# Kernel optimization log

Hardware: AMD Instinct MI355X
Metric: run time of the kernel (lower is better)

The kernel has to match this reference:

```python
import jax, jax.numpy as jnp
import numpy as np

N_NODES = 50000
N_EDGES = 640000
IN_F, H1, H2, H3, N_CLS = 128, 128, 128, 128, 40


def setup_inputs() -> dict:
    key = jax.random.key(0)
    ks = jax.random.split(key, 16)
    def lin(k, i, o):
        bound = 1.0 / np.sqrt(i)
        kw, kb = jax.random.split(k)
        W = jax.random.uniform(kw, (i, o), jnp.float32, -bound, bound)
        b = jax.random.uniform(kb, (o,), jnp.float32, -bound, bound)
        return W, b
    Wr, br = lin(ks[0], IN_F, H3)
    W1, b1 = lin(ks[1], IN_F, H1)
    W2, b2 = lin(ks[2], H1, H2)
    W3, b3 = lin(ks[3], H2, H3)
    Wop, bop = lin(ks[4], H3, N_CLS)
    x = jax.random.normal(ks[5], (N_NODES, IN_F), jnp.float32)
    src = jax.random.randint(ks[6], (N_EDGES,), 0, N_NODES, jnp.int64)
    dst = jax.random.randint(ks[7], (N_EDGES,), 0, N_NODES, jnp.int64)
    edge_weight = jax.random.uniform(ks[8], (N_EDGES,), jnp.float32)
    return {"x": x, "src": src, "dst": dst, "edge_weight": edge_weight,
            "Wr": Wr, "br": br, "W1": W1, "b1": b1, "W2": W2, "b2": b2,
            "W3": W3, "b3": b3, "Wop": Wop, "bop": bop}


def _gconv(x, src, dst, ew, W, b, n_nodes):
    # gather neighbor features, scale by edge weight, scatter-sum to dst, linear
    msg = x[src] * ew[:, None]                      # [E, d_in]
    agg = jax.ops.segment_sum(msg, dst, num_segments=n_nodes)  # [N, d_in]
    return agg @ W + b


def reference(x, src, dst, edge_weight, Wr, br, W1, b1, W2, b2, W3, b3, Wop, bop):
    n = x.shape[0]
    res = x @ Wr + br
    h = jax.nn.relu(_gconv(x, src, dst, edge_weight, W1, b1, n))
    h = jax.nn.relu(_gconv(h, src, dst, edge_weight, W2, b2, n))
    h = _gconv(h, src, dst, edge_weight, W3, b3, n)
    h = jax.nn.relu(h + res)
    return h @ Wop + bop
```

## Files before the change

### kernel.cpp

```cpp
#include <hip/hip_runtime.h>
#include <hip/hip_fp16.h>
#include <stdint.h>


#define NF 128

typedef unsigned short u16;
typedef unsigned int u32;
typedef __attribute__((ext_vector_type(8))) short short8;
typedef __attribute__((ext_vector_type(4))) float f32x4;

__device__ __forceinline__ float bf2f(u16 v) {
    union { unsigned u; float f; } x; x.u = (unsigned)v << 16; return x.f;
}
__device__ __forceinline__ u16 f2bf(float f) {
    union { float f; unsigned u; } x; x.f = f;
    unsigned r = (x.u + 0x7FFFu + ((x.u >> 16) & 1u)) >> 16;
    return (u16)r;
}


__global__ __launch_bounds__(256) void hist_rank(
    const int* __restrict__ dst, int* __restrict__ counts,
    int* __restrict__ rank, int n_edges)
{
    int e = blockIdx.x * 256 + threadIdx.x;
    if (e < n_edges) rank[e] = atomicAdd(&counts[dst[e]], 1);
}

__global__ __launch_bounds__(256) void scan_pass1(
    const int* __restrict__ counts, int* __restrict__ bsums, int n)
{
    __shared__ int s[256];
    int i = blockIdx.x * 256 + threadIdx.x;
    s[threadIdx.x] = (i < n) ? counts[i] : 0;
    __syncthreads();
    for (int off = 128; off > 0; off >>= 1) {
        if (threadIdx.x < off) s[threadIdx.x] += s[threadIdx.x + off];
        __syncthreads();
    }
    if (threadIdx.x == 0) bsums[blockIdx.x] = s[0];
}

__global__ __launch_bounds__(256) void scan_pass2(int* __restrict__ bsums, int G)
{
    __shared__ int s[256];
    int t = threadIdx.x;
    int v = (t < G) ? bsums[t] : 0;
    s[t] = v;
    __syncthreads();
    for (int off = 1; off < 256; off <<= 1) {
        int u = (t >= off) ? s[t - off] : 0;
        __syncthreads();
        s[t] += u;
        __syncthreads();
    }
    if (t < G) bsums[t] = s[t] - v;
    if (t == 0) bsums[G] = s[255];
}

__global__ __launch_bounds__(256) void scan_pass3(
    int* __restrict__ rowptr, const int* __restrict__ bsums, int n, int G)
{
    __shared__ int s[256];
    int t = threadIdx.x;
    int i = blockIdx.x * 256 + t;
    int v = (i < n) ? rowptr[i] : 0;
    s[t] = v;
    __syncthreads();
    for (int off = 1; off < 256; off <<= 1) {
        int u = (t >= off) ? s[t - off] : 0;
        __syncthreads();
        s[t] += u;
        __syncthreads();
    }
    int excl = s[t] - v + bsums[blockIdx.x];
    if (i < n) rowptr[i] = excl;
    if (i == 0) rowptr[n] = bsums[G];
}

__global__ __launch_bounds__(256) void fill_packed(
    const int* __restrict__ src, const int* __restrict__ dst,
    const float* __restrict__ ew, const int* __restrict__ rowptr,
    const int* __restrict__ rank, u32* __restrict__ ppairs, int n_edges)
{
    int e = blockIdx.x * 256 + threadIdx.x;
    if (e >= n_edges) return;
    int pos = rowptr[dst[e]] + rank[e];
    ppairs[pos] = ((u32)src[e] << 16) |
                  (u32)__half_as_ushort(__float2half_rn(ew[e]));
}


__global__ __launch_bounds__(256) void cast_x_bf16(
    const float* __restrict__ in, u16* __restrict__ out, int n_elem)
{
    int idx = (blockIdx.x * 256 + threadIdx.x) * 4;
    if (idx >= n_elem) return;
    float4 v = *reinterpret_cast<const float4*>(in + idx);
    ushort4 o;
    o.x = f2bf(v.x); o.y = f2bf(v.y); o.z = f2bf(v.z); o.w = f2bf(v.w);
    *reinterpret_cast<ushort4*>(out + idx) = o;
}

__global__ __launch_bounds__(256) void prep_weights(
    const float* __restrict__ Wr, const float* __restrict__ W1,
    const float* __restrict__ W2, const float* __restrict__ W3,
    const float* __restrict__ Wop, u16* __restrict__ Wt, u16* __restrict__ Wtop)
{
    int i = blockIdx.x * 256 + threadIdx.x;
    if (i < 4 * 16384) {
        int w = i >> 14, r = i & 16383;
        int nn = r >> 7, kk = r & 127;
        const float* W = (w == 0) ? Wr : (w == 1) ? W1 : (w == 2) ? W2 : W3;
        Wt[i] = f2bf(W[kk * NF + nn]);
    } else {
        int r = i - 4 * 16384;
        if (r < 48 * 128) {
            int nn = r >> 7, kk = r & 127;
            Wtop[r] = (nn < 40) ? f2bf(Wop[kk * 40 + nn]) : (u16)0;
        }
    }
}

__global__ __launch_bounds__(256) void agg_gather_b(
    const u16* __restrict__ xb, const int* __restrict__ rowptr,
    const u32* __restrict__ ppairs, u16* __restrict__ aggb, int n_nodes)
{
    int gid = blockIdx.x * 256 + threadIdx.x;
    int node = gid >> 4;
    if (node >= n_nodes) return;
    int f = (gid & 15) << 3;
    int e0 = rowptr[node];
    int e1 = rowptr[node + 1];
    float acc[8];
    #pragma unroll
    for (int j = 0; j < 8; j++) acc[j] = 0.f;

    int e = e0;
    for (; e + 4 <= e1; e += 4) {
        u32 p0 = ppairs[e + 0];
        u32 p1 = ppairs[e + 1];
        u32 p2 = ppairs[e + 2];
        u32 p3 = ppairs[e + 3];
        short8 v0 = *reinterpret_cast<const short8*>(xb + (size_t)(p0 >> 16) * NF + f);
        short8 v1 = *reinterpret_cast<const short8*>(xb + (size_t)(p1 >> 16) * NF + f);
        short8 v2 = *reinterpret_cast<const short8*>(xb + (size_t)(p2 >> 16) * NF + f);
        short8 v3 = *reinterpret_cast<const short8*>(xb + (size_t)(p3 >> 16) * NF + f);
        float w0 = __half2float(__ushort_as_half((u16)(p0 & 0xFFFFu)));
        float w1 = __half2float(__ushort_as_half((u16)(p1 & 0xFFFFu)));
        float w2 = __half2float(__ushort_as_half((u16)(p2 & 0xFFFFu)));
        float w3 = __half2float(__ushort_as_half((u16)(p3 & 0xFFFFu)));
        #pragma unroll
        for (int j = 0; j < 8; j++) {
            acc[j] = fmaf(bf2f((u16)v0[j]), w0, acc[j]);
            acc[j] = fmaf(bf2f((u16)v1[j]), w1, acc[j]);
            acc[j] = fmaf(bf2f((u16)v2[j]), w2, acc[j]);
            acc[j] = fmaf(bf2f((u16)v3[j]), w3, acc[j]);
        }
    }
    for (; e < e1; ++e) {
        u32 p = ppairs[e];
        float w = __half2float(__ushort_as_half((u16)(p & 0xFFFFu)));
        short8 v = *reinterpret_cast<const short8*>(xb + (size_t)(p >> 16) * NF + f);
        #pragma unroll
        for (int j = 0; j < 8; j++)
            acc[j] = fmaf(bf2f((u16)v[j]), w, acc[j]);
    }

    short8 o;
    #pragma unroll
    for (int j = 0; j < 8; j++) o[j] = (short)f2bf(acc[j]);
    *reinterpret_cast<short8*>(aggb + (size_t)node * NF + f) = o;
}

template<int RELU, int RES>
__global__ __launch_bounds__(256) void gemm_mfma128(
    const u16* __restrict__ A, const u16* __restrict__ Wt,
    const float* __restrict__ bias, const u16* __restrict__ resid,
    u16* __restrict__ out, int nrows)
{
    __shared__ u16 Bs[128 * 128];
    const int tid = threadIdx.x;
    #pragma unroll
    for (int i = 0; i < 8; i++) {
        int G = tid + i * 256;
        int row = G >> 4, g = G & 15, gs = g ^ (row & 7);
        *reinterpret_cast<short8*>(&Bs[row * NF + gs * 8]) =
            *reinterpret_cast<const short8*>(Wt + (size_t)G * 8);
    }

    const int wave = tid >> 6, lane = tid & 63;
    const int lrow = lane & 15, lk = lane >> 4;
    const int row0 = blockIdx.x * 64 + wave * 16;
    const int grow = row0 + lrow;

    short8 a[4];
    if (grow < nrows) {
        const u16* Ar = A + (size_t)grow * NF + lk * 8;
        #pragma unroll
        for (int t = 0; t < 4; t++)
            a[t] = *reinterpret_cast<const short8*>(Ar + t * 32);
    } else {
        #pragma unroll
        for (int t = 0; t < 4; t++)
            #pragma unroll
            for (int j = 0; j < 8; j++) a[t][j] = 0;
    }
    __syncthreads();

    f32x4 acc[8];
    #pragma unroll
    for (int c = 0; c < 8; c++) { acc[c][0]=0.f; acc[c][1]=0.f; acc[c][2]=0.f; acc[c][3]=0.f; }

    #pragma unroll
    for (int t = 0; t < 4; t++) {
        #pragma unroll
        for (int c = 0; c < 8; c++) {
            int col = c * 16 + lrow;
            int g = t * 4 + lk, gs = g ^ (col & 7);
            short8 b = *reinterpret_cast<const short8*>(&Bs[col * NF + gs * 8]);
            acc[c] = __builtin_amdgcn_mfma_f32_16x16x32_bf16(a[t], b, acc[c], 0, 0, 0);
        }
    }

    #pragma unroll
    for (int c = 0; c < 8; c++) {
        int col = c * 16 + lrow;
        float bv = bias[col];
        #pragma unroll
        for (int r = 0; r < 4; r++) {
            int orow = row0 + lk * 4 + r;
            if (orow < nrows) {
                float v = acc[c][r] + bv;
                if (RES) v += bf2f(resid[(size_t)orow * NF + col]);
                if (RELU) v = fmaxf(v, 0.f);
                out[(size_t)orow * NF + col] = f2bf(v);
            }
        }
    }
}

__global__ __launch_bounds__(256) void gemm_out40_mfma(
    const u16* __restrict__ H, const u16* __restrict__ Wtop,
    const float* __restrict__ bop, float* __restrict__ out, int nrows)
{
    __shared__ u16 Bs[48 * 128];
    const int tid = threadIdx.x;
    #pragma unroll
    for (int i = 0; i < 3; i++) {
        int G = tid + i * 256;
        int row = G >> 4, g = G & 15, gs = g ^ (row & 7);
        *reinterpret_cast<short8*>(&Bs[row * NF + gs * 8]) =
            *reinterpret_cast<const short8*>(Wtop + (size_t)G * 8);
    }

    const int wave = tid >> 6, lane = tid & 63;
    const int lrow = lane & 15, lk = lane >> 4;
    const int row0 = blockIdx.x * 64 + wave * 16;
    const int grow = row0 + lrow;

    short8 a[4];
    if (grow < nrows) {
        const u16* Hr = H + (size_t)grow * NF + lk * 8;
        #pragma unroll
        for (int t = 0; t < 4; t++)
            a[t] = *reinterpret_cast<const short8*>(Hr + t * 32);
    } else {
        #pragma unroll
        for (int t = 0; t < 4; t++)
            #pragma unroll
            for (int j = 0; j < 8; j++) a[t][j] = 0;
    }
    __syncthreads();

    f32x4 acc[3];
    #pragma unroll
    for (int c = 0; c < 3; c++) { acc[c][0]=0.f; acc[c][1]=0.f; acc[c][2]=0.f; acc[c][3]=0.f; }

    #pragma unroll
    for (int t = 0; t < 4; t++) {
        #pragma unroll
        for (int c = 0; c < 3; c++) {
            int col = c * 16 + lrow;
            int g = t * 4 + lk, gs = g ^ (col & 7);
            short8 b = *reinterpret_cast<const short8*>(&Bs[col * NF + gs * 8]);
            acc[c] = __builtin_amdgcn_mfma_f32_16x16x32_bf16(a[t], b, acc[c], 0, 0, 0);
        }
    }

    #pragma unroll
    for (int c = 0; c < 3; c++) {
        int col = c * 16 + lrow;
        if (col < 40) {
            float bv = bop[col];
            #pragma unroll
            for (int r = 0; r < 4; r++) {
                int orow = row0 + lk * 4 + r;
                if (orow < nrows)
                    out[(size_t)orow * 40 + col] = acc[c][r] + bv;
            }
        }
    }
}


extern "C" void kernel_launch(void* const* d_in, const int* in_sizes, int n_in,
                              void* d_out, int out_size, void* d_ws, size_t ws_size,
                              hipStream_t stream)
{
    const float* x   = (const float*)d_in[0];
    const int*   src = (const int*)d_in[1];
    const int*   dst = (const int*)d_in[2];
    const float* ew  = (const float*)d_in[3];
    const float* Wr  = (const float*)d_in[4];
    const float* br  = (const float*)d_in[5];
    const float* W1  = (const float*)d_in[6];
    const float* b1  = (const float*)d_in[7];
    const float* W2  = (const float*)d_in[8];
    const float* b2  = (const float*)d_in[9];
    const float* W3  = (const float*)d_in[10];
    const float* b3  = (const float*)d_in[11];
    const float* Wop = (const float*)d_in[12];
    const float* bop = (const float*)d_in[13];
    float* out = (float*)d_out;

    const int n_nodes = in_sizes[0] / NF;
    const int n_edges = in_sizes[1];
    const size_t feat = (size_t)n_nodes * NF;

    u16* xb   = (u16*)d_ws;
    u16* hb   = xb + feat;
    u16* aggb = hb + feat;
    u16* resb = aggb + feat;
    u16* Wt   = resb + feat;
    u16* Wtop = Wt + 4 * 16384;
    int* rowptr = (int*)(Wtop + 48 * 128);
    const int G1 = (n_nodes + 255) / 256;
    int* bsums  = rowptr + (n_nodes + 1);
    int* rank   = bsums + (G1 + 1);
    u32* ppairs = (u32*)(rank + n_edges);

    const int edge_grid = (n_edges + 255) / 256;
    const int gemm_grid = (n_nodes + 63) / 64;
    const int agg_grid  = (n_nodes * 16 + 255) / 256;
    const int castx_grid = ((int)feat / 4 + 255) / 256;

    hipMemsetAsync(rowptr, 0, (size_t)(n_nodes + 1) * sizeof(int), stream);
    hist_rank<<<edge_grid, 256, 0, stream>>>(dst, rowptr, rank, n_edges);
    scan_pass1<<<G1, 256, 0, stream>>>(rowptr, bsums, n_nodes);
    scan_pass2<<<1, 256, 0, stream>>>(bsums, G1);
    scan_pass3<<<G1, 256, 0, stream>>>(rowptr, bsums, n_nodes, G1);
    fill_packed<<<edge_grid, 256, 0, stream>>>(src, dst, ew, rowptr, rank, ppairs, n_edges);

    cast_x_bf16<<<castx_grid, 256, 0, stream>>>(x, xb, (int)feat);
    prep_weights<<<(4 * 16384 + 48 * 128 + 255) / 256, 256, 0, stream>>>(
        Wr, W1, W2, W3, Wop, Wt, Wtop);

    gemm_mfma128<0, 0><<<gemm_grid, 256, 0, stream>>>(xb, Wt, br, nullptr, resb, n_nodes);

    agg_gather_b<<<agg_grid, 256, 0, stream>>>(xb, rowptr, ppairs, aggb, n_nodes);
    gemm_mfma128<1, 0><<<gemm_grid, 256, 0, stream>>>(aggb, Wt + 16384, b1, nullptr, hb, n_nodes);

    agg_gather_b<<<agg_grid, 256, 0, stream>>>(hb, rowptr, ppairs, aggb, n_nodes);
    gemm_mfma128<1, 0><<<gemm_grid, 256, 0, stream>>>(aggb, Wt + 2 * 16384, b2, nullptr, hb, n_nodes);

    agg_gather_b<<<agg_grid, 256, 0, stream>>>(hb, rowptr, ppairs, aggb, n_nodes);
    gemm_mfma128<1, 1><<<gemm_grid, 256, 0, stream>>>(aggb, Wt + 3 * 16384, b3, resb, hb, n_nodes);

    gemm_out40_mfma<<<gemm_grid, 256, 0, stream>>>(hb, Wtop, bop, out, n_nodes);
}
```

Before: 198.5 us.

## Fuse prep kernels, pad CSR rows to multiples of four, vectorize gather, 128-row GEMM blocks

Merges histogram, x cast and weight prep into one launch and folds scan passes 2 and 3 into one kernel, cutting kernel launches. CSR rows are padded to multiples of four with zeroed edge pairs, so the gather kernel can use 16-byte vector index loads and issue eight feature loads per iteration with no scalar tail. The GEMM kernels now handle 128 rows per block and reuse the staged weight tile across two sub-tiles. The costs are an extra memset of the padded edge buffer, and padding edges that point at node 0 with zero weight.

```diff
diff --git a/kernel.cpp b/kernel.cpp
--- a/kernel.cpp
+++ b/kernel.cpp
@@ -19,13 +19,42 @@
     return (u16)r;
 }
 
-
-__global__ __launch_bounds__(256) void hist_rank(
-    const int* __restrict__ dst, int* __restrict__ counts,
-    int* __restrict__ rank, int n_edges)
-{
-    int e = blockIdx.x * 256 + threadIdx.x;
-    if (e < n_edges) rank[e] = atomicAdd(&counts[dst[e]], 1);
+__global__ __launch_bounds__(256) void prep_all(
+    const int* __restrict__ dst, int* __restrict__ counts, int* __restrict__ rank,
+    int n_edges,
+    const float* __restrict__ x, u16* __restrict__ xb, int n_feat,
+    const float* __restrict__ Wr, const float* __restrict__ W1,
+    const float* __restrict__ W2, const float* __restrict__ W3,
+    const float* __restrict__ Wop, u16* __restrict__ Wt, u16* __restrict__ Wtop,
+    int HB, int CB)
+{
+    int b = blockIdx.x;
+    if (b < HB) {
+        int e = b * 256 + threadIdx.x;
+        if (e < n_edges) rank[e] = atomicAdd(&counts[dst[e]], 1);
+    } else if (b < HB + CB) {
+        int idx = ((b - HB) * 256 + threadIdx.x) * 4;
+        if (idx < n_feat) {
+            float4 v = *reinterpret_cast<const float4*>(x + idx);
+            ushort4 o;
+            o.x = f2bf(v.x); o.y = f2bf(v.y); o.z = f2bf(v.z); o.w = f2bf(v.w);
+            *reinterpret_cast<ushort4*>(xb + idx) = o;
+        }
+    } else {
+        int i = (b - HB - CB) * 256 + threadIdx.x;
+        if (i < 4 * 16384) {
+            int w = i >> 14, r = i & 16383;
+            int nn = r >> 7, kk = r & 127;
+            const float* W = (w == 0) ? Wr : (w == 1) ? W1 : (w == 2) ? W2 : W3;
+            Wt[i] = f2bf(W[kk * NF + nn]);
+        } else {
+            int r = i - 4 * 16384;
+            if (r < 48 * 128) {
+                int nn = r >> 7, kk = r & 127;
+                Wtop[r] = (nn < 40) ? f2bf(Wop[kk * 40 + nn]) : (u16)0;
+            }
+        }
+    }
 }
 
 __global__ __launch_bounds__(256) void scan_pass1(
@@ -33,7 +62,8 @@
 {
     __shared__ int s[256];
     int i = blockIdx.x * 256 + threadIdx.x;
-    s[threadIdx.x] = (i < n) ? counts[i] : 0;
+    int c = (i < n) ? counts[i] : 0;
+    s[threadIdx.x] = (c + 3) & ~3;
     __syncthreads();
     for (int off = 128; off > 0; off >>= 1) {
         if (threadIdx.x < off) s[threadIdx.x] += s[threadIdx.x + off];
@@ -42,12 +72,13 @@
     if (threadIdx.x == 0) bsums[blockIdx.x] = s[0];
 }
 
-__global__ __launch_bounds__(256) void scan_pass2(int* __restrict__ bsums, int G)
+__global__ __launch_bounds__(256) void scan_pass23(
+    int* __restrict__ rowptr, const int* __restrict__ bsums, int n, int G)
 {
     __shared__ int s[256];
     int t = threadIdx.x;
-    int v = (t < G) ? bsums[t] : 0;
-    s[t] = v;
+    int bv = (t < G) ? bsums[t] : 0;
+    s[t] = bv;
     __syncthreads();
     for (int off = 1; off < 256; off <<= 1) {
         int u = (t >= off) ? s[t - off] : 0;
@@ -55,17 +86,13 @@
         s[t] += u;
         __syncthreads();
     }
-    if (t < G) bsums[t] = s[t] - v;
-    if (t == 0) bsums[G] = s[255];
-}
-
-__global__ __launch_bounds__(256) void scan_pass3(
-    int* __restrict__ rowptr, const int* __restrict__ bsums, int n, int G)
-{
-    __shared__ int s[256];
-    int t = threadIdx.x;
+    int blockoff = (blockIdx.x > 0) ? s[blockIdx.x - 1] : 0;
+    int total = s[255];
+    __syncthreads();
+
     int i = blockIdx.x * 256 + t;
-    int v = (i < n) ? rowptr[i] : 0;
+    int c = (i < n) ? rowptr[i] : 0;
+    int v = (c + 3) & ~3;
     s[t] = v;
     __syncthreads();
     for (int off = 1; off < 256; off <<= 1) {
@@ -74,9 +101,9 @@
         s[t] += u;
         __syncthreads();
     }
-    int excl = s[t] - v + bsums[blockIdx.x];
+    int excl = s[t] - v + blockoff;
     if (i < n) rowptr[i] = excl;
-    if (i == 0) rowptr[n] = bsums[G];
+    if (i == 0) rowptr[n] = total;
 }
 
 __global__ __launch_bounds__(256) void fill_packed(
@@ -89,38 +116,6 @@
     int pos = rowptr[dst[e]] + rank[e];
     ppairs[pos] = ((u32)src[e] << 16) |
                   (u32)__half_as_ushort(__float2half_rn(ew[e]));
-}
-
-
-__global__ __launch_bounds__(256) void cast_x_bf16(
-    const float* __restrict__ in, u16* __restrict__ out, int n_elem)
-{
-    int idx = (blockIdx.x * 256 + threadIdx.x) * 4;
-    if (idx >= n_elem) return;
-    float4 v = *reinterpret_cast<const float4*>(in + idx);
-    ushort4 o;
-    o.x = f2bf(v.x); o.y = f2bf(v.y); o.z = f2bf(v.z); o.w = f2bf(v.w);
-    *reinterpret_cast<ushort4*>(out + idx) = o;
-}
-
-__global__ __launch_bounds__(256) void prep_weights(
-    const float* __restrict__ Wr, const float* __restrict__ W1,
-    const float* __restrict__ W2, const float* __restrict__ W3,
-    const float* __restrict__ Wop, u16* __restrict__ Wt, u16* __restrict__ Wtop)
-{
-    int i = blockIdx.x * 256 + threadIdx.x;
-    if (i < 4 * 16384) {
-        int w = i >> 14, r = i & 16383;
-        int nn = r >> 7, kk = r & 127;
-        const float* W = (w == 0) ? Wr : (w == 1) ? W1 : (w == 2) ? W2 : W3;
-        Wt[i] = f2bf(W[kk * NF + nn]);
-    } else {
-        int r = i - 4 * 16384;
-        if (r < 48 * 128) {
-            int nn = r >> 7, kk = r & 127;
-            Wtop[r] = (nn < 40) ? f2bf(Wop[kk * 40 + nn]) : (u16)0;
-        }
-    }
 }
 
 __global__ __launch_bounds__(256) void agg_gather_b(
@@ -133,39 +128,43 @@
     int f = (gid & 15) << 3;
     int e0 = rowptr[node];
     int e1 = rowptr[node + 1];
+    const u16* xf = xb + f;
+
     float acc[8];
     #pragma unroll
     for (int j = 0; j < 8; j++) acc[j] = 0.f;
 
     int e = e0;
-    for (; e + 4 <= e1; e += 4) {
-        u32 p0 = ppairs[e + 0];
-        u32 p1 = ppairs[e + 1];
-        u32 p2 = ppairs[e + 2];
-        u32 p3 = ppairs[e + 3];
-        short8 v0 = *reinterpret_cast<const short8*>(xb + (size_t)(p0 >> 16) * NF + f);
-        short8 v1 = *reinterpret_cast<const short8*>(xb + (size_t)(p1 >> 16) * NF + f);
-        short8 v2 = *reinterpret_cast<const short8*>(xb + (size_t)(p2 >> 16) * NF + f);
-        short8 v3 = *reinterpret_cast<const short8*>(xb + (size_t)(p3 >> 16) * NF + f);
-        float w0 = __half2float(__ushort_as_half((u16)(p0 & 0xFFFFu)));
-        float w1 = __half2float(__ushort_as_half((u16)(p1 & 0xFFFFu)));
-        float w2 = __half2float(__ushort_as_half((u16)(p2 & 0xFFFFu)));
-        float w3 = __half2float(__ushort_as_half((u16)(p3 & 0xFFFFu)));
-        #pragma unroll
-        for (int j = 0; j < 8; j++) {
-            acc[j] = fmaf(bf2f((u16)v0[j]), w0, acc[j]);
-            acc[j] = fmaf(bf2f((u16)v1[j]), w1, acc[j]);
-            acc[j] = fmaf(bf2f((u16)v2[j]), w2, acc[j]);
-            acc[j] = fmaf(bf2f((u16)v3[j]), w3, acc[j]);
-        }
-    }
-    for (; e < e1; ++e) {
-        u32 p = ppairs[e];
-        float w = __half2float(__ushort_as_half((u16)(p & 0xFFFFu)));
-        short8 v = *reinterpret_cast<const short8*>(xb + (size_t)(p >> 16) * NF + f);
-        #pragma unroll
-        for (int j = 0; j < 8; j++)
-            acc[j] = fmaf(bf2f((u16)v[j]), w, acc[j]);
+    for (; e + 8 <= e1; e += 8) {
+        uint4 pa = *reinterpret_cast<const uint4*>(ppairs + e);
+        uint4 pb = *reinterpret_cast<const uint4*>(ppairs + e + 4);
+        u32 p[8] = {pa.x, pa.y, pa.z, pa.w, pb.x, pb.y, pb.z, pb.w};
+        short8 v[8];
+        #pragma unroll
+        for (int k = 0; k < 8; k++)
+            v[k] = *reinterpret_cast<const short8*>(xf + (size_t)(p[k] >> 16) * NF);
+        #pragma unroll
+        for (int k = 0; k < 8; k++) {
+            float w = __half2float(__ushort_as_half((u16)(p[k] & 0xFFFFu)));
+            #pragma unroll
+            for (int j = 0; j < 8; j++)
+                acc[j] = fmaf(bf2f((u16)v[k][j]), w, acc[j]);
+        }
+    }
+    if (e < e1) {
+        uint4 pa = *reinterpret_cast<const uint4*>(ppairs + e);
+        u32 p[4] = {pa.x, pa.y, pa.z, pa.w};
+        short8 v[4];
+        #pragma unroll
+        for (int k = 0; k < 4; k++)
+            v[k] = *reinterpret_cast<const short8*>(xf + (size_t)(p[k] >> 16) * NF);
+        #pragma unroll
+        for (int k = 0; k < 4; k++) {
+            float w = __half2float(__ushort_as_half((u16)(p[k] & 0xFFFFu)));
+            #pragma unroll
+            for (int j = 0; j < 8; j++)
+                acc[j] = fmaf(bf2f((u16)v[k][j]), w, acc[j]);
+        }
     }
 
     short8 o;
@@ -189,53 +188,57 @@
         *reinterpret_cast<short8*>(&Bs[row * NF + gs * 8]) =
             *reinterpret_cast<const short8*>(Wt + (size_t)G * 8);
     }
+    __syncthreads();
 
     const int wave = tid >> 6, lane = tid & 63;
     const int lrow = lane & 15, lk = lane >> 4;
-    const int row0 = blockIdx.x * 64 + wave * 16;
-    const int grow = row0 + lrow;
-
-    short8 a[4];
-    if (grow < nrows) {
-        const u16* Ar = A + (size_t)grow * NF + lk * 8;
-        #pragma unroll
-        for (int t = 0; t < 4; t++)
-            a[t] = *reinterpret_cast<const short8*>(Ar + t * 32);
-    } else {
-        #pragma unroll
-        for (int t = 0; t < 4; t++)
-            #pragma unroll
-            for (int j = 0; j < 8; j++) a[t][j] = 0;
-    }
-    __syncthreads();
-
-    f32x4 acc[8];
-    #pragma unroll
-    for (int c = 0; c < 8; c++) { acc[c][0]=0.f; acc[c][1]=0.f; acc[c][2]=0.f; acc[c][3]=0.f; }
-
-    #pragma unroll
-    for (int t = 0; t < 4; t++) {
+
+    #pragma unroll
+    for (int sub = 0; sub < 2; ++sub) {
+        const int row0 = blockIdx.x * 128 + sub * 64 + wave * 16;
+        const int grow = row0 + lrow;
+
+        short8 a[4];
+        if (grow < nrows) {
+            const u16* Ar = A + (size_t)grow * NF + lk * 8;
+            #pragma unroll
+            for (int t = 0; t < 4; t++)
+                a[t] = *reinterpret_cast<const short8*>(Ar + t * 32);
+        } else {
+            #pragma unroll
+            for (int t = 0; t < 4; t++)
+                #pragma unroll
+                for (int j = 0; j < 8; j++) a[t][j] = 0;
+        }
+
+        f32x4 acc[8];
+        #pragma unroll
+        for (int c = 0; c < 8; c++) { acc[c][0]=0.f; acc[c][1]=0.f; acc[c][2]=0.f; acc[c][3]=0.f; }
+
+        #pragma unroll
+        for (int t = 0; t < 4; t++) {
+            #pragma unroll
+            for (int c = 0; c < 8; c++) {
+                int col = c * 16 + lrow;
+                int g = t * 4 + lk, gs = g ^ (col & 7);
+                short8 b = *reinterpret_cast<const short8*>(&Bs[col * NF + gs * 8]);
+                acc[c] = __builtin_amdgcn_mfma_f32_16x16x32_bf16(a[t], b, acc[c], 0, 0, 0);
+            }
+        }
+
         #pragma unroll
         for (int c = 0; c < 8; c++) {
             int col = c * 16 + lrow;
-            int g = t * 4 + lk, gs = g ^ (col & 7);
-            short8 b = *reinterpret_cast<const short8*>(&Bs[col * NF + gs * 8]);
-            acc[c] = __builtin_amdgcn_mfma_f32_16x16x32_bf16(a[t], b, acc[c], 0, 0, 0);
-        }
-    }
-
-    #pragma unroll
-    for (int c = 0; c < 8; c++) {
-        int col = c * 16 + lrow;
-        float bv = bias[col];
-        #pragma unroll
-        for (int r = 0; r < 4; r++) {
-            int orow = row0 + lk * 4 + r;
-            if (orow < nrows) {
-                float v = acc[c][r] + bv;
-                if (RES) v += bf2f(resid[(size_t)orow * NF + col]);
-                if (RELU) v = fmaxf(v, 0.f);
-                out[(size_t)orow * NF + col] = f2bf(v);
+            float bv = bias[col];
+            #pragma unroll
+            for (int r = 0; r < 4; r++) {
+                int orow = row0 + lk * 4 + r;
+                if (orow < nrows) {
+                    float v = acc[c][r] + bv;
+                    if (RES) v += bf2f(resid[(size_t)orow * NF + col]);
+                    if (RELU) v = fmaxf(v, 0.f);
+                    out[(size_t)orow * NF + col] = f2bf(v);
+                }
             }
         }
     }
@@ -254,51 +257,55 @@
         *reinterpret_cast<short8*>(&Bs[row * NF + gs * 8]) =
             *reinterpret_cast<const short8*>(Wtop + (size_t)G * 8);
     }
+    __syncthreads();
 
     const int wave = tid >> 6, lane = tid & 63;
     const int lrow = lane & 15, lk = lane >> 4;
-    const int row0 = blockIdx.x * 64 + wave * 16;
-    const int grow = row0 + lrow;
-
-    short8 a[4];
-    if (grow < nrows) {
-        const u16* Hr = H + (size_t)grow * NF + lk * 8;
-        #pragma unroll
-        for (int t = 0; t < 4; t++)
-            a[t] = *reinterpret_cast<const short8*>(Hr + t * 32);
-    } else {
-        #pragma unroll
-        for (int t = 0; t < 4; t++)
-            #pragma unroll
-            for (int j = 0; j < 8; j++) a[t][j] = 0;
-    }
-    __syncthreads();
-
-    f32x4 acc[3];
-    #pragma unroll
-    for (int c = 0; c < 3; c++) { acc[c][0]=0.f; acc[c][1]=0.f; acc[c][2]=0.f; acc[c][3]=0.f; }
-
-    #pragma unroll
-    for (int t = 0; t < 4; t++) {
+
+    #pragma unroll
+    for (int sub = 0; sub < 2; ++sub) {
+        const int row0 = blockIdx.x * 128 + sub * 64 + wave * 16;
+        const int grow = row0 + lrow;
+
+        short8 a[4];
+        if (grow < nrows) {
+            const u16* Hr = H + (size_t)grow * NF + lk * 8;
+            #pragma unroll
+            for (int t = 0; t < 4; t++)
+                a[t] = *reinterpret_cast<const short8*>(Hr + t * 32);
+        } else {
+            #pragma unroll
+            for (int t = 0; t < 4; t++)
+                #pragma unroll
+                for (int j = 0; j < 8; j++) a[t][j] = 0;
+        }
+
+        f32x4 acc[3];
+        #pragma unroll
+        for (int c = 0; c < 3; c++) { acc[c][0]=0.f; acc[c][1]=0.f; acc[c][2]=0.f; acc[c][3]=0.f; }
+
+        #pragma unroll
+        for (int t = 0; t < 4; t++) {
+            #pragma unroll
+            for (int c = 0; c < 3; c++) {
+                int col = c * 16 + lrow;
+                int g = t * 4 + lk, gs = g ^ (col & 7);
+                short8 b = *reinterpret_cast<const short8*>(&Bs[col * NF + gs * 8]);
+                acc[c] = __builtin_amdgcn_mfma_f32_16x16x32_bf16(a[t], b, acc[c], 0, 0, 0);
+            }
+        }
+
         #pragma unroll
         for (int c = 0; c < 3; c++) {
             int col = c * 16 + lrow;
-            int g = t * 4 + lk, gs = g ^ (col & 7);
-            short8 b = *reinterpret_cast<const short8*>(&Bs[col * NF + gs * 8]);
-            acc[c] = __builtin_amdgcn_mfma_f32_16x16x32_bf16(a[t], b, acc[c], 0, 0, 0);
-        }
-    }
-
-    #pragma unroll
-    for (int c = 0; c < 3; c++) {
-        int col = c * 16 + lrow;
-        if (col < 40) {
-            float bv = bop[col];
-            #pragma unroll
-            for (int r = 0; r < 4; r++) {
-                int orow = row0 + lk * 4 + r;
-                if (orow < nrows)
-                    out[(size_t)orow * 40 + col] = acc[c][r] + bv;
+            if (col < 40) {
+                float bv = bop[col];
+                #pragma unroll
+                for (int r = 0; r < 4; r++) {
+                    int orow = row0 + lk * 4 + r;
+                    if (orow < nrows)
+                        out[(size_t)orow * 40 + col] = acc[c][r] + bv;
+                }
             }
         }
     }
@@ -328,6 +335,7 @@
     const int n_nodes = in_sizes[0] / NF;
     const int n_edges = in_sizes[1];
     const size_t feat = (size_t)n_nodes * NF;
+    const int padded_cap = n_edges + 3 * n_nodes + 8;
 
     u16* xb   = (u16*)d_ws;
     u16* hb   = xb + feat;
@@ -339,23 +347,22 @@
     const int G1 = (n_nodes + 255) / 256;
     int* bsums  = rowptr + (n_nodes + 1);
     int* rank   = bsums + (G1 + 1);
-    u32* ppairs = (u32*)(rank + n_edges);
-
-    const int edge_grid = (n_edges + 255) / 256;
-    const int gemm_grid = (n_nodes + 63) / 64;
+    u32* ppairs = (u32*)(((uintptr_t)(rank + n_edges) + 15) & ~(uintptr_t)15);
+
+    const int HB = (n_edges + 255) / 256;
+    const int CB = ((int)feat / 4 + 255) / 256;
+    const int PB = (4 * 16384 + 48 * 128 + 255) / 256;
+    const int gemm_grid = (n_nodes + 127) / 128;
     const int agg_grid  = (n_nodes * 16 + 255) / 256;
-    const int castx_grid = ((int)feat / 4 + 255) / 256;
 
     hipMemsetAsync(rowptr, 0, (size_t)(n_nodes + 1) * sizeof(int), stream);
-    hist_rank<<<edge_grid, 256, 0, stream>>>(dst, rowptr, rank, n_edges);
+    hipMemsetAsync(ppairs, 0, (size_t)padded_cap * sizeof(u32), stream);
+    prep_all<<<HB + CB + PB, 256, 0, stream>>>(
+        dst, rowptr, rank, n_edges, x, xb, (int)feat,
+        Wr, W1, W2, W3, Wop, Wt, Wtop, HB, CB);
     scan_pass1<<<G1, 256, 0, stream>>>(rowptr, bsums, n_nodes);
-    scan_pass2<<<1, 256, 0, stream>>>(bsums, G1);
-    scan_pass3<<<G1, 256, 0, stream>>>(rowptr, bsums, n_nodes, G1);
-    fill_packed<<<edge_grid, 256, 0, stream>>>(src, dst, ew, rowptr, rank, ppairs, n_edges);
-
-    cast_x_bf16<<<castx_grid, 256, 0, stream>>>(x, xb, (int)feat);
-    prep_weights<<<(4 * 16384 + 48 * 128 + 255) / 256, 256, 0, stream>>>(
-        Wr, W1, W2, W3, Wop, Wt, Wtop);
+    scan_pass23<<<G1, 256, 0, stream>>>(rowptr, bsums, n_nodes, G1);
+    fill_packed<<<HB, 256, 0, stream>>>(src, dst, ew, rowptr, rank, ppairs, n_edges);
 
     gemm_mfma128<0, 0><<<gemm_grid, 256, 0, stream>>>(xb, Wt, br, nullptr, resb, n_nodes);
 
```

New measurement: 199.2 us. No clear change (+0.3%).
